# Kernel tuning notes

Hardware: AMD Instinct MI355X
Metric: run time of the kernel (lower is better)

The kernel has to match this reference:

```python
import jax, jax.numpy as jnp
import numpy as np


def setup_inputs() -> dict:
    key = jax.random.key(0)
    k1, k2, k3 = jax.random.split(key, 3)
    B, C, D, S = 16, 80, 1024, 14  # batch, num_classes, feature dim, conv size
    return {
        "batch_size": B,
        "img_feature_map": jax.random.normal(k1, (B, D, S, S), dtype=jnp.float32),
        "word_features": jax.random.normal(k2, (C, D), dtype=jnp.float32),
        "fc_a_w": jax.random.normal(k3, (D,), dtype=jnp.float32) / np.float32(np.sqrt(D)),
        "fc_a_b": jnp.zeros((), dtype=jnp.float32),
    }


def reference(batch_size, img_feature_map, word_features, fc_a_w, fc_a_b):
    # img_feature_map: [B, D, H, W] -> [B, H, W, D]
    img = jnp.transpose(img_feature_map, (0, 2, 3, 1))
    # class-wise gated feature: tanh(img * word) -> [B, H, W, C, D]
    gated = jnp.tanh(img[:, :, :, None, :] * word_features[None, None, None, :, :])
    # rank-1 linear score: [B, H, W, C]
    scores = jnp.einsum('bhwcd,d->bhwc', gated, fc_a_w) + fc_a_b
    B, H, W, C = scores.shape
    # softmax over spatial positions (H*W) per (batch, class)
    coef = jax.nn.softmax(scores.reshape(B, H * W, C), axis=1).reshape(B, H, W, C)
    # attention-weighted spatial pooling -> [B, C, D]
    return jnp.einsum('bhwc,bhwd->bcd', coef, img)
```

## Files before the change

kernel.cpp:

```cpp
#include <hip/hip_runtime.h>

#define BB 16
#define CC 80
#define DD 1024
#define HW 196
#define NSP (BB * HW)
#define NCH 8
#define DCH 128
#define CPB 4
#define NCQ (CC / CPB)
#define PCPB 8
#define TWO_LOG2E 2.8853900817779268f

__global__ __launch_bounds__(256) void scores_k(const float* __restrict__ img,
                                                const float* __restrict__ word,
                                                const float* __restrict__ fa,
                                                float* __restrict__ partial,
                                                float* __restrict__ imgT) {
    const int g = blockIdx.x * 256 + threadIdx.x;
    if (g >= NSP) return;
    const int b  = g / HW;
    const int hw = g - b * HW;
    const int d0 = blockIdx.y * DCH;
    const int c0 = blockIdx.z * CPB;

    const float* ip = img + ((size_t)b * DD + d0) * HW + hw;

    float p[CPB];
#pragma unroll
    for (int k = 0; k < CPB; ++k) p[k] = 0.f;

    for (int q = 0; q < DCH / 32; ++q) {
        float iv[32];
        const float* qp = ip + (size_t)q * 32 * HW;
#pragma unroll
        for (int i = 0; i < 32; ++i)
            iv[i] = qp[(size_t)i * HW];

        if (blockIdx.z == 0) {
            float4* tp = (float4*)(imgT + (size_t)g * DD + d0 + q * 32);
#pragma unroll
            for (int i = 0; i < 8; ++i)
                tp[i] = make_float4(iv[4 * i], iv[4 * i + 1], iv[4 * i + 2], iv[4 * i + 3]);
        }

#pragma unroll
        for (int i = 0; i < 32; ++i)
            iv[i] *= TWO_LOG2E;

        const float* fp = fa + d0 + q * 32;
#pragma unroll
        for (int k = 0; k < CPB; ++k) {
            const float* wp = word + (size_t)(c0 + k) * DD + d0 + q * 32;
            float p0 = 0.f, p1 = 0.f;
#pragma unroll
            for (int i = 0; i < 32; i += 2) {
                float y0 = iv[i]     * wp[i];
                float y1 = iv[i + 1] * wp[i + 1];
                float e0 = __builtin_amdgcn_exp2f(y0);
                float e1 = __builtin_amdgcn_exp2f(y1);
                float r0 = __builtin_amdgcn_rcpf(e0 + 1.f);
                float r1 = __builtin_amdgcn_rcpf(e1 + 1.f);
                p0 = fmaf(fp[i],     r0, p0);
                p1 = fmaf(fp[i + 1], r1, p1);
            }
            p[k] += p0 + p1;
        }
    }

#pragma unroll
    for (int k = 0; k < CPB; ++k)
        partial[(((size_t)b * NCH + blockIdx.y) * CC + (c0 + k)) * HW + hw]
            = (-TWO_LOG2E) * p[k];
}

__global__ __launch_bounds__(256) void softmax_k(float* partial) {
    const int idx = blockIdx.x * 4 + (threadIdx.x >> 6);
    const int l   = threadIdx.x & 63;
    const int b   = idx / CC;
    const int c   = idx - b * CC;

    float x0 = 0.f, x1 = 0.f, x2 = 0.f, x3 = 0.f;
#pragma unroll
    for (int ch = 0; ch < NCH; ++ch) {
        const float* pp = partial + (((size_t)b * NCH + ch) * CC + c) * HW;
        x0 += pp[l];
        x1 += pp[l + 64];
        x2 += pp[l + 128];
        if (l < HW - 192) x3 += pp[l + 192];
    }
    float x3m = (l < HW - 192) ? x3 : -3.4e38f;

    float m = fmaxf(fmaxf(x0, x1), fmaxf(x2, x3m));
#pragma unroll
    for (int off = 32; off >= 1; off >>= 1) m = fmaxf(m, __shfl_xor(m, off, 64));

    float e0 = __builtin_amdgcn_exp2f(x0 - m);
    float e1 = __builtin_amdgcn_exp2f(x1 - m);
    float e2 = __builtin_amdgcn_exp2f(x2 - m);
    float e3 = (l < HW - 192) ? __builtin_amdgcn_exp2f(x3 - m) : 0.f;

    float s = (e0 + e1) + (e2 + e3);
#pragma unroll
    for (int off = 32; off >= 1; off >>= 1) s += __shfl_xor(s, off, 64);

    float inv = __builtin_amdgcn_rcpf(s);
    float* cr = partial + (((size_t)b * NCH) * CC + c) * HW;
    cr[l]       = e0 * inv;
    cr[l + 64]  = e1 * inv;
    cr[l + 128] = e2 * inv;
    if (l < HW - 192) cr[l + 192] = e3 * inv;
}

__global__ __launch_bounds__(128) void pool3_k(const float* __restrict__ imgT,
                                               const float* __restrict__ coef,
                                               float* __restrict__ out) {
    const int b  = blockIdx.x;
    const int d  = blockIdx.y * 128 + threadIdx.x;
    const int c0 = blockIdx.z * PCPB;

    const float* ib = imgT + (size_t)b * HW * DD + d;
    const float* cb = coef + (((size_t)b * NCH) * CC + c0) * HW;

    float acc[PCPB];
#pragma unroll
    for (int k = 0; k < PCPB; ++k) acc[k] = 0.f;

#pragma unroll 7
    for (int h = 0; h < HW; h += 4) {
        float i0 = ib[(size_t)(h    ) * DD];
        float i1 = ib[(size_t)(h + 1) * DD];
        float i2 = ib[(size_t)(h + 2) * DD];
        float i3 = ib[(size_t)(h + 3) * DD];
#pragma unroll
        for (int k = 0; k < PCPB; ++k) {
            float4 cv = *(const float4*)(cb + (size_t)k * HW + h);
            acc[k] = fmaf(cv.x, i0, fmaf(cv.y, i1, fmaf(cv.z, i2, fmaf(cv.w, i3, acc[k]))));
        }
    }

    float* ob = out + ((size_t)b * CC + c0) * DD + d;
#pragma unroll
    for (int k = 0; k < PCPB; ++k)
        ob[(size_t)k * DD] = acc[k];
}

extern "C" void kernel_launch(void* const* d_in, const int* in_sizes, int n_in,
                              void* d_out, int out_size, void* d_ws, size_t ws_size,
                              hipStream_t stream) {
    const float* img  = (const float*)d_in[1];
    const float* word = (const float*)d_in[2];
    const float* fa   = (const float*)d_in[3];
    float* out = (float*)d_out;

    float* partial = (float*)d_ws;
    float* imgT    = partial + (size_t)BB * NCH * CC * HW;

    scores_k<<<dim3((NSP + 255) / 256, NCH, NCQ), 256, 0, stream>>>(img, word, fa, partial, imgT);
    softmax_k<<<dim3(BB * CC / 4), 256, 0, stream>>>(partial);
    pool3_k<<<dim3(BB, DD / 128, CC / PCPB), 128, 0, stream>>>(imgT, partial, out);
}
```

Before: 168.4 us.

## Fuse softmax into pooling kernel with shared-memory coefficients and float4 D tiles

Removes the separate softmax kernel. The pooling kernel now reduces the partial scores across D-chunks, runs the softmax in-block and stages the coefficients in shared memory, then accumulates with each thread covering 4 consecutive D values via float4 loads. The scores kernel also doubles classes per block (CPB 4->8), halving redundant image reads at the cost of more registers. The fused pool grid has only 160 blocks, far fewer than before, and each block redoes the softmax for its own classes.

```diff
diff --git a/kernel.cpp b/kernel.cpp
--- a/kernel.cpp
+++ b/kernel.cpp
@@ -7,7 +7,7 @@
 #define NSP (BB * HW)
 #define NCH 8
 #define DCH 128
-#define CPB 4
+#define CPB 8
 #define NCQ (CC / CPB)
 #define PCPB 8
 #define TWO_LOG2E 2.8853900817779268f
@@ -74,75 +74,78 @@
             = (-TWO_LOG2E) * p[k];
 }
 
-__global__ __launch_bounds__(256) void softmax_k(float* partial) {
-    const int idx = blockIdx.x * 4 + (threadIdx.x >> 6);
-    const int l   = threadIdx.x & 63;
-    const int b   = idx / CC;
-    const int c   = idx - b * CC;
+__global__ __launch_bounds__(256) void pool4_k(const float* __restrict__ imgT,
+                                               const float* __restrict__ partial,
+                                               float* __restrict__ out) {
+    __shared__ float ct[PCPB * HW];
+    const int b  = blockIdx.x;
+    const int cg = blockIdx.y * PCPB;
+    const int t  = threadIdx.x;
+    const int w  = t >> 6, l = t & 63;
 
-    float x0 = 0.f, x1 = 0.f, x2 = 0.f, x3 = 0.f;
 #pragma unroll
-    for (int ch = 0; ch < NCH; ++ch) {
-        const float* pp = partial + (((size_t)b * NCH + ch) * CC + c) * HW;
-        x0 += pp[l];
-        x1 += pp[l + 64];
-        x2 += pp[l + 128];
-        if (l < HW - 192) x3 += pp[l + 192];
+    for (int cc = 0; cc < 2; ++cc) {
+        const int o = w + 4 * cc;
+        const int c = cg + o;
+
+        float x0 = 0.f, x1 = 0.f, x2 = 0.f, x3 = 0.f;
+#pragma unroll
+        for (int ch = 0; ch < NCH; ++ch) {
+            const float* pp = partial + (((size_t)b * NCH + ch) * CC + c) * HW;
+            x0 += pp[l];
+            x1 += pp[l + 64];
+            x2 += pp[l + 128];
+            if (l < HW - 192) x3 += pp[l + 192];
+        }
+        float x3m = (l < HW - 192) ? x3 : -3.4e38f;
+
+        float m = fmaxf(fmaxf(x0, x1), fmaxf(x2, x3m));
+#pragma unroll
+        for (int off = 32; off >= 1; off >>= 1) m = fmaxf(m, __shfl_xor(m, off, 64));
+
+        float e0 = __builtin_amdgcn_exp2f(x0 - m);
+        float e1 = __builtin_amdgcn_exp2f(x1 - m);
+        float e2 = __builtin_amdgcn_exp2f(x2 - m);
+        float e3 = (l < HW - 192) ? __builtin_amdgcn_exp2f(x3 - m) : 0.f;
+
+        float s = (e0 + e1) + (e2 + e3);
+#pragma unroll
+        for (int off = 32; off >= 1; off >>= 1) s += __shfl_xor(s, off, 64);
+
+        float inv = __builtin_amdgcn_rcpf(s);
+        float* cr = ct + o * HW;
+        cr[l]       = e0 * inv;
+        cr[l + 64]  = e1 * inv;
+        cr[l + 128] = e2 * inv;
+        if (l < HW - 192) cr[l + 192] = e3 * inv;
     }
-    float x3m = (l < HW - 192) ? x3 : -3.4e38f;
+    __syncthreads();
 
-    float m = fmaxf(fmaxf(x0, x1), fmaxf(x2, x3m));
+    const float* ib = imgT + (size_t)b * HW * DD + 4 * t;
+
+    float4 acc[PCPB];
 #pragma unroll
-    for (int off = 32; off >= 1; off >>= 1) m = fmaxf(m, __shfl_xor(m, off, 64));
+    for (int k = 0; k < PCPB; ++k) acc[k] = make_float4(0.f, 0.f, 0.f, 0.f);
 
-    float e0 = __builtin_amdgcn_exp2f(x0 - m);
-    float e1 = __builtin_amdgcn_exp2f(x1 - m);
-    float e2 = __builtin_amdgcn_exp2f(x2 - m);
-    float e3 = (l < HW - 192) ? __builtin_amdgcn_exp2f(x3 - m) : 0.f;
-
-    float s = (e0 + e1) + (e2 + e3);
-#pragma unroll
-    for (int off = 32; off >= 1; off >>= 1) s += __shfl_xor(s, off, 64);
-
-    float inv = __builtin_amdgcn_rcpf(s);
-    float* cr = partial + (((size_t)b * NCH) * CC + c) * HW;
-    cr[l]       = e0 * inv;
-    cr[l + 64]  = e1 * inv;
-    cr[l + 128] = e2 * inv;
-    if (l < HW - 192) cr[l + 192] = e3 * inv;
-}
-
-__global__ __launch_bounds__(128) void pool3_k(const float* __restrict__ imgT,
-                                               const float* __restrict__ coef,
-                                               float* __restrict__ out) {
-    const int b  = blockIdx.x;
-    const int d  = blockIdx.y * 128 + threadIdx.x;
-    const int c0 = blockIdx.z * PCPB;
-
-    const float* ib = imgT + (size_t)b * HW * DD + d;
-    const float* cb = coef + (((size_t)b * NCH) * CC + c0) * HW;
-
-    float acc[PCPB];
-#pragma unroll
-    for (int k = 0; k < PCPB; ++k) acc[k] = 0.f;
-
-#pragma unroll 7
+#pragma unroll 2
     for (int h = 0; h < HW; h += 4) {
-        float i0 = ib[(size_t)(h    ) * DD];
-        float i1 = ib[(size_t)(h + 1) * DD];
-        float i2 = ib[(size_t)(h + 2) * DD];
-        float i3 = ib[(size_t)(h + 3) * DD];
+        float4 i0 = *(const float4*)(ib + (size_t)(h    ) * DD);
+        float4 i1 = *(const float4*)(ib + (size_t)(h + 1) * DD);
+        float4 i2 = *(const float4*)(ib + (size_t)(h + 2) * DD);
+        float4 i3 = *(const float4*)(ib + (size_t)(h + 3) * DD);
 #pragma unroll
         for (int k = 0; k < PCPB; ++k) {
-            float4 cv = *(const float4*)(cb + (size_t)k * HW + h);
-            acc[k] = fmaf(cv.x, i0, fmaf(cv.y, i1, fmaf(cv.z, i2, fmaf(cv.w, i3, acc[k]))));
+            float4 cv = *(const float4*)(ct + k * HW + h);
+            acc[k].x = fmaf(cv.x, i0.x, fmaf(cv.y, i1.x, fmaf(cv.z, i2.x, fmaf(cv.w, i3.x, acc[k].x))));
+            acc[k].y = fmaf(cv.x, i0.y, fmaf(cv.y, i1.y, fmaf(cv.z, i2.y, fmaf(cv.w, i3.y, acc[k].y))));
+            acc[k].z = fmaf(cv.x, i0.z, fmaf(cv.y, i1.z, fmaf(cv.z, i2.z, fmaf(cv.w, i3.z, acc[k].z))));
+            acc[k].w = fmaf(cv.x, i0.w, fmaf(cv.y, i1.w, fmaf(cv.z, i2.w, fmaf(cv.w, i3.w, acc[k].w))));
         }
     }
 
-    float* ob = out + ((size_t)b * CC + c0) * DD + d;
 #pragma unroll
     for (int k = 0; k < PCPB; ++k)
-        ob[(size_t)k * DD] = acc[k];
+        *(float4*)(out + ((size_t)b * CC + cg + k) * DD + 4 * t) = acc[k];
 }
 
 extern "C" void kernel_launch(void* const* d_in, const int* in_sizes, int n_in,
@@ -157,6 +160,5 @@
     float* imgT    = partial + (size_t)BB * NCH * CC * HW;
 
     scores_k<<<dim3((NSP + 255) / 256, NCH, NCQ), 256, 0, stream>>>(img, word, fa, partial, imgT);
-    softmax_k<<<dim3(BB * CC / 4), 256, 0, stream>>>(partial);
-    pool3_k<<<dim3(BB, DD / 128, CC / PCPB), 128, 0, stream>>>(imgT, partial, out);
+    pool4_k<<<dim3(BB, CC / PCPB), 256, 0, stream>>>(imgT, partial, out);
 }
```

New measurement: 173.3 us. +2.9%, slower.

## Stage coefficients in LDS and widen pooling tile to 40 classes per thread

Applied to the files above, without the earlier changes.

Replaces the pooling kernel with one that loads a 40-class slab of softmax coefficients into shared memory and has each thread accumulate all 40 classes for one feature column. Image loads are software-prefetched one 8-row step ahead. This cuts the number of re-reads of the transposed image from ten to two, but it launches only 128 blocks and uses many registers per thread, which risks underfilling the GPU. The workspace order of the two buffers is also swapped.

```diff
diff --git a/kernel.cpp b/kernel.cpp
--- a/kernel.cpp
+++ b/kernel.cpp
@@ -9,7 +9,7 @@
 #define DCH 128
 #define CPB 4
 #define NCQ (CC / CPB)
-#define PCPB 8
+#define PCC 40
 #define TWO_LOG2E 2.8853900817779268f
 
 __global__ __launch_bounds__(256) void scores_k(const float* __restrict__ img,
@@ -112,36 +112,74 @@
     if (l < HW - 192) cr[l + 192] = e3 * inv;
 }
 
-__global__ __launch_bounds__(128) void pool3_k(const float* __restrict__ imgT,
+__global__ __launch_bounds__(256) void pool5_k(const float* __restrict__ imgT,
                                                const float* __restrict__ coef,
                                                float* __restrict__ out) {
-    const int b  = blockIdx.x;
-    const int d  = blockIdx.y * 128 + threadIdx.x;
-    const int c0 = blockIdx.z * PCPB;
-
-    const float* ib = imgT + (size_t)b * HW * DD + d;
-    const float* cb = coef + (((size_t)b * NCH) * CC + c0) * HW;
-
-    float acc[PCPB];
-#pragma unroll
-    for (int k = 0; k < PCPB; ++k) acc[k] = 0.f;
-
-#pragma unroll 7
-    for (int h = 0; h < HW; h += 4) {
-        float i0 = ib[(size_t)(h    ) * DD];
-        float i1 = ib[(size_t)(h + 1) * DD];
-        float i2 = ib[(size_t)(h + 2) * DD];
-        float i3 = ib[(size_t)(h + 3) * DD];
-#pragma unroll
-        for (int k = 0; k < PCPB; ++k) {
-            float4 cv = *(const float4*)(cb + (size_t)k * HW + h);
-            acc[k] = fmaf(cv.x, i0, fmaf(cv.y, i1, fmaf(cv.z, i2, fmaf(cv.w, i3, acc[k]))));
-        }
-    }
-
-    float* ob = out + ((size_t)b * CC + c0) * DD + d;
-#pragma unroll
-    for (int k = 0; k < PCPB; ++k)
+    __shared__ float ct[PCC][200];
+    const int b   = blockIdx.x;
+    const int dt0 = blockIdx.y * 256;
+    const int c0  = blockIdx.z * PCC;
+    const int t   = threadIdx.x;
+
+    const float* cbase = coef + ((size_t)b * NCH * CC + c0) * HW;
+#pragma unroll
+    for (int i = 0; i < 8; ++i) {
+        int idx = t + i * 256;
+        if (idx < (PCC * HW) / 4) {
+            int c = idx / (HW / 4);
+            int r = (idx - c * (HW / 4)) * 4;
+            *(float4*)&ct[c][r] = *(const float4*)(cbase + (size_t)idx * 4);
+        }
+    }
+    __syncthreads();
+
+    const float* ib = imgT + (size_t)b * HW * DD + dt0 + t;
+
+    float acc[PCC];
+#pragma unroll
+    for (int k = 0; k < PCC; ++k) acc[k] = 0.f;
+
+    float iv[8];
+#pragma unroll
+    for (int j = 0; j < 8; ++j) iv[j] = ib[(size_t)j * DD];
+
+    for (int h = 0; h < 192; h += 8) {
+        float nv[8];
+#pragma unroll
+        for (int j = 0; j < 8; ++j)
+            nv[j] = ib[(size_t)(h + 8 + j) * DD];
+#pragma unroll
+        for (int k = 0; k < PCC; ++k) {
+            float4 cA = *(const float4*)&ct[k][h];
+            float4 cB = *(const float4*)&ct[k][h + 4];
+            float a = acc[k];
+            a = fmaf(cA.x, iv[0], a);
+            a = fmaf(cA.y, iv[1], a);
+            a = fmaf(cA.z, iv[2], a);
+            a = fmaf(cA.w, iv[3], a);
+            a = fmaf(cB.x, iv[4], a);
+            a = fmaf(cB.y, iv[5], a);
+            a = fmaf(cB.z, iv[6], a);
+            a = fmaf(cB.w, iv[7], a);
+            acc[k] = a;
+        }
+#pragma unroll
+        for (int j = 0; j < 8; ++j) iv[j] = nv[j];
+    }
+#pragma unroll
+    for (int k = 0; k < PCC; ++k) {
+        float4 cA = *(const float4*)&ct[k][192];
+        float a = acc[k];
+        a = fmaf(cA.x, iv[0], a);
+        a = fmaf(cA.y, iv[1], a);
+        a = fmaf(cA.z, iv[2], a);
+        a = fmaf(cA.w, iv[3], a);
+        acc[k] = a;
+    }
+
+    float* ob = out + ((size_t)b * CC + c0) * DD + dt0 + t;
+#pragma unroll
+    for (int k = 0; k < PCC; ++k)
         ob[(size_t)k * DD] = acc[k];
 }
 
@@ -153,10 +191,10 @@
     const float* fa   = (const float*)d_in[3];
     float* out = (float*)d_out;
 
-    float* partial = (float*)d_ws;
-    float* imgT    = partial + (size_t)BB * NCH * CC * HW;
+    float* imgT    = (float*)d_ws;
+    float* partial = imgT + (size_t)NSP * DD;
 
     scores_k<<<dim3((NSP + 255) / 256, NCH, NCQ), 256, 0, stream>>>(img, word, fa, partial, imgT);
     softmax_k<<<dim3(BB * CC / 4), 256, 0, stream>>>(partial);
-    pool3_k<<<dim3(BB, DD / 128, CC / PCPB), 128, 0, stream>>>(imgT, partial, out);
-}
+    pool5_k<<<dim3(BB, DD / 256, CC / PCC), 256, 0, stream>>>(imgT, partial, out);
+}
```

Result: slower. 182.3 us (+8.3%).

## Retile pooling kernel with shared-memory coefficient tile and 4x4 register blocking

Applied to the files above, without the earlier changes.

The pooling kernel is rewritten so each block stages a 196x16 coefficient tile in LDS, transposed so each position holds the coefficients for all its classes. Each thread then computes a 4-class by 4-feature register tile using float4 loads of imgT and the coefficients. The goal is more FMAs per load and fewer redundant global coefficient reads. The cost is fewer blocks (16x4x5 = 320), an extra __syncthreads with a serial LDS fill per block, and possible LDS bank conflicts on the transposed writes.

```diff
diff --git a/kernel.cpp b/kernel.cpp
--- a/kernel.cpp
+++ b/kernel.cpp
@@ -9,7 +9,6 @@
 #define DCH 128
 #define CPB 4
 #define NCQ (CC / CPB)
-#define PCPB 8
 #define TWO_LOG2E 2.8853900817779268f
 
 __global__ __launch_bounds__(256) void scores_k(const float* __restrict__ img,
@@ -112,37 +111,59 @@
     if (l < HW - 192) cr[l + 192] = e3 * inv;
 }
 
-__global__ __launch_bounds__(128) void pool3_k(const float* __restrict__ imgT,
+__global__ __launch_bounds__(256) void pool6_k(const float* __restrict__ imgT,
                                                const float* __restrict__ coef,
                                                float* __restrict__ out) {
+    __shared__ float ct[HW][16];
     const int b  = blockIdx.x;
-    const int d  = blockIdx.y * 128 + threadIdx.x;
-    const int c0 = blockIdx.z * PCPB;
+    const int dq = blockIdx.y * 256;
+    const int cq = blockIdx.z * 16;
+    const int t  = threadIdx.x;
 
-    const float* ib = imgT + (size_t)b * HW * DD + d;
-    const float* cb = coef + (((size_t)b * NCH) * CC + c0) * HW;
+    for (int idx = t; idx < 16 * HW; idx += 256) {
+        const int c = idx / HW;
+        const int h = idx - c * HW;
+        ct[h][c] = coef[(((size_t)b * NCH) * CC + cq + c) * HW + h];
+    }
+    __syncthreads();
 
-    float acc[PCPB];
-#pragma unroll
-    for (int k = 0; k < PCPB; ++k) acc[k] = 0.f;
+    const int cg = t >> 6;
+    const int dg = t & 63;
+    const float* ib = imgT + (size_t)b * HW * DD + dq + 4 * dg;
+    const float* cp = &ct[0][4 * cg];
 
-#pragma unroll 7
-    for (int h = 0; h < HW; h += 4) {
-        float i0 = ib[(size_t)(h    ) * DD];
-        float i1 = ib[(size_t)(h + 1) * DD];
-        float i2 = ib[(size_t)(h + 2) * DD];
-        float i3 = ib[(size_t)(h + 3) * DD];
-#pragma unroll
-        for (int k = 0; k < PCPB; ++k) {
-            float4 cv = *(const float4*)(cb + (size_t)k * HW + h);
-            acc[k] = fmaf(cv.x, i0, fmaf(cv.y, i1, fmaf(cv.z, i2, fmaf(cv.w, i3, acc[k]))));
-        }
+    float4 a0 = make_float4(0.f, 0.f, 0.f, 0.f);
+    float4 a1 = make_float4(0.f, 0.f, 0.f, 0.f);
+    float4 a2 = make_float4(0.f, 0.f, 0.f, 0.f);
+    float4 a3 = make_float4(0.f, 0.f, 0.f, 0.f);
+
+#pragma unroll 4
+    for (int h = 0; h < HW; ++h) {
+        const float4 iv = *(const float4*)(ib + (size_t)h * DD);
+        const float4 cv = *(const float4*)(cp + h * 16);
+        a0.x = fmaf(cv.x, iv.x, a0.x);
+        a0.y = fmaf(cv.x, iv.y, a0.y);
+        a0.z = fmaf(cv.x, iv.z, a0.z);
+        a0.w = fmaf(cv.x, iv.w, a0.w);
+        a1.x = fmaf(cv.y, iv.x, a1.x);
+        a1.y = fmaf(cv.y, iv.y, a1.y);
+        a1.z = fmaf(cv.y, iv.z, a1.z);
+        a1.w = fmaf(cv.y, iv.w, a1.w);
+        a2.x = fmaf(cv.z, iv.x, a2.x);
+        a2.y = fmaf(cv.z, iv.y, a2.y);
+        a2.z = fmaf(cv.z, iv.z, a2.z);
+        a2.w = fmaf(cv.z, iv.w, a2.w);
+        a3.x = fmaf(cv.w, iv.x, a3.x);
+        a3.y = fmaf(cv.w, iv.y, a3.y);
+        a3.z = fmaf(cv.w, iv.z, a3.z);
+        a3.w = fmaf(cv.w, iv.w, a3.w);
     }
 
-    float* ob = out + ((size_t)b * CC + c0) * DD + d;
-#pragma unroll
-    for (int k = 0; k < PCPB; ++k)
-        ob[(size_t)k * DD] = acc[k];
+    float* ob = out + (((size_t)b * CC + cq + 4 * cg) * DD) + dq + 4 * dg;
+    *(float4*)(ob)                  = a0;
+    *(float4*)(ob + (size_t)DD)     = a1;
+    *(float4*)(ob + (size_t)2 * DD) = a2;
+    *(float4*)(ob + (size_t)3 * DD) = a3;
 }
 
 extern "C" void kernel_launch(void* const* d_in, const int* in_sizes, int n_in,
@@ -158,5 +179,5 @@
 
     scores_k<<<dim3((NSP + 255) / 256, NCH, NCQ), 256, 0, stream>>>(img, word, fa, partial, imgT);
     softmax_k<<<dim3(BB * CC / 4), 256, 0, stream>>>(partial);
-    pool3_k<<<dim3(BB, DD / 128, CC / PCPB), 128, 0, stream>>>(imgT, partial, out);
+    pool6_k<<<dim3(BB, DD / 256, CC / 16), 256, 0, stream>>>(imgT, partial, out);
 }
```

Result: faster. 159.3 us (-5.4%).
